# Performance work log

Hardware: AMD Instinct MI355X
Metric: run time of the kernel (lower is better)

The kernel has to match this reference:

```python
import jax, jax.numpy as jnp
import numpy as np

L = 2          # n_layer
H = 8          # n_head
DM = 512       # d_model
DFF = 2048     # d_ff
DH = DM // H   # head dim (query_dimensions)
M = DH         # Favor n_dims random features
B, S = 1, 2048
EPS = 1e-6     # causal linear attention eps
LN_EPS = 1e-5  # torch LayerNorm default


def setup_inputs() -> dict:
    key = jax.random.key(0)
    ks = jax.random.split(key, 12)
    sc = 0.02
    d = {}
    d['x'] = jax.random.normal(ks[0], (B, S, DM), dtype=jnp.float32)
    for i, (n, shape) in enumerate([('Wq', (L, DM, DM)), ('Wk', (L, DM, DM)),
                                    ('Wv', (L, DM, DM)), ('Wo', (L, DM, DM)),
                                    ('W1', (L, DM, DFF)), ('W2', (L, DFF, DM))]):
        d[n] = jax.random.normal(ks[i + 1], shape, dtype=jnp.float32) * sc
    d['bq'] = jnp.zeros((L, DM), jnp.float32)
    d['bk'] = jnp.zeros((L, DM), jnp.float32)
    d['bv'] = jnp.zeros((L, DM), jnp.float32)
    d['bo'] = jnp.zeros((L, DM), jnp.float32)
    d['b1'] = jnp.zeros((L, DFF), jnp.float32)
    d['b2'] = jnp.zeros((L, DM), jnp.float32)
    d['g1'] = jnp.ones((L, DM), jnp.float32)
    d['be1'] = jnp.zeros((L, DM), jnp.float32)
    d['g2'] = jnp.ones((L, DM), jnp.float32)
    d['be2'] = jnp.zeros((L, DM), jnp.float32)
    # FAVOR+ random projection matrix per layer: [Dh, M]
    d['omega'] = jax.random.normal(ks[7], (L, DH, M), dtype=jnp.float32)
    return d


def _favor(x, omega):
    # x: [B,S,H,Dh]; softmax_temp = 1/sqrt(Dh) applied as x * sqrt(temp)
    xs = x * (DH ** -0.25)
    nrm = jnp.sum(xs * xs, axis=-1, keepdims=True)       # [B,S,H,1]
    u = jnp.einsum('bshd,dm->bshm', xs, omega)           # [B,S,H,M]
    return jnp.exp(u - 0.5 * nrm) * (M ** -0.5)


def _ln(x, g, b):
    mu = jnp.mean(x, -1, keepdims=True)
    var = jnp.mean((x - mu) ** 2, -1, keepdims=True)
    return (x - mu) * jax.lax.rsqrt(var + LN_EPS) * g + b


def _forward(x, Wq, bq, Wk, bk, Wv, bv, Wo, bo, omega,
             W1, b1, W2, b2, g1, be1, g2, be2):
    out = x
    for l in range(L):
        q = (out @ Wq[l] + bq[l]).reshape(B, S, H, DH)
        k = (out @ Wk[l] + bk[l]).reshape(B, S, H, DH)
        v = (out @ Wv[l] + bv[l]).reshape(B, S, H, DH)
        pq = _favor(q, omega[l])
        pk = _favor(k, omega[l])
        # causal linear attention: running sums of phi(k) v^T and phi(k)
        kv = jnp.cumsum(jnp.einsum('bshm,bshd->bshmd', pk, v), axis=1)  # [B,S,H,M,Dh]
        num = jnp.einsum('bshm,bshmd->bshd', pq, kv)
        den = jnp.einsum('bshm,bshm->bsh', pq, jnp.cumsum(pk, axis=1)) + EPS
        a = (num / den[..., None]).reshape(B, S, DM)
        # post-norm encoder layer (fast-transformers TransformerEncoderLayer)
        out = out + (a @ Wo[l] + bo[l])
        out = _ln(out, g1[l], be1[l])
        y = jax.nn.relu(out @ W1[l] + b1[l]) @ W2[l] + b2[l]
        out = _ln(out + y, g2[l], be2[l])
    return out


def reference(x, Wq, bq, Wk, bk, Wv, bv, Wo, bo, omega,
              W1, b1, W2, b2, g1, be1, g2, be2):
    return _forward(x, Wq, bq, Wk, bk, Wv, bv, Wo, bo, omega,
                    W1, b1, W2, b2, g1, be1, g2, be2)
```

## Files before the change

kernel.cpp:

```cpp
#include <hip/hip_runtime.h>
#include <hip/hip_bf16.h>

#define S_  2048
#define DM_ 512
#define H_  8
#define DH_ 64
#define MF_ 64
#define DFF_ 2048
#define L_  2
#define CT_ 64
#define NC_ (S_ / CT_)
#define EPS_ 1e-6f
#define LN_EPS_ 1e-5f

#define LSW_   3145728
#define W1OFF_ 1048576
#define W2OFF_ 2097152
#define WOOFF_ 786432

typedef unsigned short ushortT;
typedef unsigned int u32;
typedef float f4 __attribute__((ext_vector_type(4)));
typedef short s8 __attribute__((ext_vector_type(8)));
typedef u32 u32x2 __attribute__((ext_vector_type(2)));

__device__ __forceinline__ ushortT f2b(float f) {
  union { float f; unsigned u; } v; v.f = f;
  unsigned r = v.u + 0x7fffu + ((v.u >> 16) & 1u);
  return (ushortT)(r >> 16);
}
__device__ __forceinline__ float bu2f(ushortT h) {
  union { unsigned u; float f; } v; v.u = ((unsigned)h) << 16; return v.f;
}
__device__ __forceinline__ u32 pk2(float a, float b) {
  return (u32)f2b(a) | ((u32)f2b(b) << 16);
}

__global__ __launch_bounds__(256) void tcast_all(
    const float* __restrict__ x,
    const float* __restrict__ Wq, const float* __restrict__ Wk,
    const float* __restrict__ Wv, const float* __restrict__ Wo,
    const float* __restrict__ W1, const float* __restrict__ W2,
    const float* __restrict__ omg,
    float* __restrict__ cur, ushortT* __restrict__ curb,
    ushortT* __restrict__ wb, ushortT* __restrict__ omgTb) {
  const int bid = blockIdx.x;
  const int t = threadIdx.x;
  if (bid >= 6152) {
    const int i = (bid - 6152) * 256 + t;
    float v = x[i];
    cur[i] = v;
    curb[i] = f2b(v);
    return;
  }
  __shared__ ushortT tile[32][33];
  const float* src; ushortT* dst; int K, N, bx, by;
  if (bid < 2048) {
    const int z = bid >> 8, widx = z & 3, lay = z >> 2;
    const float* s4[4] = {Wq, Wk, Wv, Wo};
    src = s4[widx] + (size_t)lay * DM_ * DM_;
    dst = wb + (size_t)lay * LSW_ + (size_t)widx * DM_ * DM_;
    K = DM_; N = DM_; bx = bid & 15; by = (bid >> 4) & 15;
  } else if (bid < 4096) {
    const int r = bid - 2048;
    const int lay = r >> 10;
    src = W1 + (size_t)lay * DM_ * DFF_;
    dst = wb + (size_t)lay * LSW_ + W1OFF_;
    K = DM_; N = DFF_; bx = r & 63; by = (r >> 6) & 15;
  } else if (bid < 6144) {
    const int r = bid - 4096;
    const int lay = r >> 10;
    src = W2 + (size_t)lay * DFF_ * DM_;
    dst = wb + (size_t)lay * LSW_ + W2OFF_;
    K = DFF_; N = DM_; bx = r & 15; by = (r >> 4) & 63;
  } else {
    const int r = bid - 6144;
    const int lay = r >> 2;
    src = omg + (size_t)lay * DH_ * MF_;
    dst = omgTb + (size_t)lay * DH_ * MF_;
    K = DH_; N = MF_; bx = r & 1; by = (r >> 1) & 1;
  }
  const int cc = t & 31, r0 = t >> 5;
  const int n0 = bx * 32, k0 = by * 32;
#pragma unroll
  for (int i = 0; i < 4; ++i) {
    int r = r0 + 8 * i;
    tile[r][cc] = f2b(src[(size_t)(k0 + r) * N + n0 + cc]);
  }
  __syncthreads();
#pragma unroll
  for (int i = 0; i < 4; ++i) {
    int r = r0 + 8 * i;
    dst[(size_t)(n0 + r) * K + k0 + cc] = tile[cc][r];
  }
}

template<bool RELU, bool HAS_RES, bool OUT_BF16>
__global__ __launch_bounds__(256) void mgemm(
    const ushortT* __restrict__ A, const ushortT* __restrict__ Wt,
    const float* __restrict__ bq_, const float* __restrict__ bk_,
    const float* __restrict__ bv_, const float* __restrict__ Res,
    float* __restrict__ Cf, ushortT* __restrict__ Cb, int K, int N) {
  __shared__ ushortT sA[2][2048];
  __shared__ ushortT sB[2][2048];
  const int t = threadIdx.x;
  const int w = t >> 6, l = t & 63;
  const int wm = w >> 1, wn = w & 1;
  const int n0 = blockIdx.x * 64, m0 = blockIdx.y * 64;
  const int z = blockIdx.z;
  const ushortT* Wz = Wt + (size_t)z * K * N;
  const float* bias = (z == 0) ? bq_ : (z == 1 ? bk_ : bv_);

  const int rs = w * 16 + (l >> 2);
  const int qs = (l & 3) ^ ((rs >> 1) & 3);
  const ushortT* gA = A  + (size_t)(m0 + rs) * K + qs * 8;
  const ushortT* gB = Wz + (size_t)(n0 + rs) * K + qs * 8;

  const int Ra = wm * 32 + (l & 15);
  const int Rb = wn * 32 + (l & 15);
  const int qq = l >> 4;
  const int aoff = (Ra * 4 + (qq ^ ((Ra >> 1) & 3))) * 8;
  const int boff = (Rb * 4 + (qq ^ ((Rb >> 1) & 3))) * 8;

  f4 acc[2][2];
#pragma unroll
  for (int i = 0; i < 2; ++i)
#pragma unroll
    for (int j = 0; j < 2; ++j) acc[i][j] = (f4){0.f, 0.f, 0.f, 0.f};

  auto stage = [&](int buf, int ko) {
    __builtin_amdgcn_global_load_lds(
        (const __attribute__((address_space(1))) void*)(gA + ko),
        (__attribute__((address_space(3))) void*)(&sA[buf][w * 512]), 16, 0, 0);
    __builtin_amdgcn_global_load_lds(
        (const __attribute__((address_space(1))) void*)(gB + ko),
        (__attribute__((address_space(3))) void*)(&sB[buf][w * 512]), 16, 0, 0);
  };

  stage(0, 0);
  const int nk = K >> 5;
  for (int ks = 0; ks < nk; ++ks) {
    __syncthreads();
    if (ks + 1 < nk) stage((ks + 1) & 1, (ks + 1) * 32);
    const ushortT* pa = sA[ks & 1];
    const ushortT* pb = sB[ks & 1];
    s8 a0 = *(const s8*)(pa + aoff);
    s8 a1 = *(const s8*)(pa + aoff + 512);
    s8 b0 = *(const s8*)(pb + boff);
    s8 b1 = *(const s8*)(pb + boff + 512);
    acc[0][0] = __builtin_amdgcn_mfma_f32_16x16x32_bf16(a0, b0, acc[0][0], 0, 0, 0);
    acc[0][1] = __builtin_amdgcn_mfma_f32_16x16x32_bf16(a0, b1, acc[0][1], 0, 0, 0);
    acc[1][0] = __builtin_amdgcn_mfma_f32_16x16x32_bf16(a1, b0, acc[1][0], 0, 0, 0);
    acc[1][1] = __builtin_amdgcn_mfma_f32_16x16x32_bf16(a1, b1, acc[1][1], 0, 0, 0);
  }

  const size_t outz = (size_t)z * S_ * N;
  const int colb = n0 + wn * 32 + (l & 15);
  const int rowb = m0 + wm * 32 + ((l >> 4) << 2);
#pragma unroll
  for (int mt = 0; mt < 2; ++mt) {
#pragma unroll
    for (int nt = 0; nt < 2; ++nt) {
      const int c = colb + nt * 16;
      const float bv = bias[c];
#pragma unroll
      for (int r = 0; r < 4; ++r) {
        const int rr = rowb + mt * 16 + r;
        float v = acc[mt][nt][r] + bv;
        if (HAS_RES) v += Res[(size_t)rr * N + c];
        if (RELU) v = fmaxf(v, 0.f);
        if (OUT_BF16) Cb[outz + (size_t)rr * N + c] = f2b(v);
        else          Cf[outz + (size_t)rr * N + c] = v;
      }
    }
  }
}

__global__ __launch_bounds__(256) void mgemm_part(
    const ushortT* __restrict__ A, const ushortT* __restrict__ Wt,
    float* __restrict__ PS, int K, int N, int KS) {
  __shared__ ushortT sA[2][2048];
  __shared__ ushortT sB[2][2048];
  const int t = threadIdx.x;
  const int w = t >> 6, l = t & 63;
  const int wm = w >> 1, wn = w & 1;
  const int n0 = blockIdx.x * 64, m0 = blockIdx.y * 64;
  const int z = blockIdx.z;

  const int rs = w * 16 + (l >> 2);
  const int qs = (l & 3) ^ ((rs >> 1) & 3);
  const ushortT* gA = A  + (size_t)(m0 + rs) * K + z * KS + qs * 8;
  const ushortT* gB = Wt + (size_t)(n0 + rs) * K + z * KS + qs * 8;

  const int Ra = wm * 32 + (l & 15);
  const int Rb = wn * 32 + (l & 15);
  const int qq = l >> 4;
  const int aoff = (Ra * 4 + (qq ^ ((Ra >> 1) & 3))) * 8;
  const int boff = (Rb * 4 + (qq ^ ((Rb >> 1) & 3))) * 8;

  f4 acc[2][2];
#pragma unroll
  for (int i = 0; i < 2; ++i)
#pragma unroll
    for (int j = 0; j < 2; ++j) acc[i][j] = (f4){0.f, 0.f, 0.f, 0.f};

  auto stage = [&](int buf, int ko) {
    __builtin_amdgcn_global_load_lds(
        (const __attribute__((address_space(1))) void*)(gA + ko),
        (__attribute__((address_space(3))) void*)(&sA[buf][w * 512]), 16, 0, 0);
    __builtin_amdgcn_global_load_lds(
        (const __attribute__((address_space(1))) void*)(gB + ko),
        (__attribute__((address_space(3))) void*)(&sB[buf][w * 512]), 16, 0, 0);
  };

  stage(0, 0);
  const int nk = KS >> 5;
  for (int ks = 0; ks < nk; ++ks) {
    __syncthreads();
    if (ks + 1 < nk) stage((ks + 1) & 1, (ks + 1) * 32);
    const ushortT* pa = sA[ks & 1];
    const ushortT* pb = sB[ks & 1];
    s8 a0 = *(const s8*)(pa + aoff);
    s8 a1 = *(const s8*)(pa + aoff + 512);
    s8 b0 = *(const s8*)(pb + boff);
    s8 b1 = *(const s8*)(pb + boff + 512);
    acc[0][0] = __builtin_amdgcn_mfma_f32_16x16x32_bf16(a0, b0, acc[0][0], 0, 0, 0);
    acc[0][1] = __builtin_amdgcn_mfma_f32_16x16x32_bf16(a0, b1, acc[0][1], 0, 0, 0);
    acc[1][0] = __builtin_amdgcn_mfma_f32_16x16x32_bf16(a1, b0, acc[1][0], 0, 0, 0);
    acc[1][1] = __builtin_amdgcn_mfma_f32_16x16x32_bf16(a1, b1, acc[1][1], 0, 0, 0);
  }

  float* out = PS + (size_t)z * S_ * N;
  const int colb = n0 + wn * 32 + (l & 15);
  const int rowb = m0 + wm * 32 + ((l >> 4) << 2);
#pragma unroll
  for (int mt = 0; mt < 2; ++mt) {
#pragma unroll
    for (int nt = 0; nt < 2; ++nt) {
      const int c = colb + nt * 16;
#pragma unroll
      for (int r = 0; r < 4; ++r)
        out[(size_t)(rowb + mt * 16 + r) * N + c] = acc[mt][nt][r];
    }
  }
}

__global__ __launch_bounds__(256) void redln(const float* __restrict__ PS, int nsplit,
                                             const float* __restrict__ bias,
                                             const float* __restrict__ res,
                                             const float* __restrict__ g,
                                             const float* __restrict__ be,
                                             float* __restrict__ outF,
                                             ushortT* __restrict__ outB) {
  const int s = blockIdx.x, t = threadIdx.x;
  float v0 = bias[t] + res[(size_t)s * DM_ + t];
  float v1 = bias[t + 256] + res[(size_t)s * DM_ + 256 + t];
  for (int z = 0; z < nsplit; ++z) {
    const float* p = PS + (size_t)z * S_ * DM_ + (size_t)s * DM_;
    v0 += p[t];
    v1 += p[256 + t];
  }
  float sum = v0 + v1, sq = v0 * v0 + v1 * v1;
  for (int off = 32; off > 0; off >>= 1) {
    sum += __shfl_down(sum, off);
    sq += __shfl_down(sq, off);
  }
  __shared__ float ssum[4], ssq[4];
  __shared__ float smean, srstd;
  const int w = t >> 6;
  if ((t & 63) == 0) { ssum[w] = sum; ssq[w] = sq; }
  __syncthreads();
  if (t == 0) {
    float S1 = ssum[0] + ssum[1] + ssum[2] + ssum[3];
    float S2 = ssq[0] + ssq[1] + ssq[2] + ssq[3];
    float mu = S1 / DM_;
    smean = mu;
    srstd = rsqrtf(S2 / DM_ - mu * mu + LN_EPS_);
  }
  __syncthreads();
  const float mu = smean, rs = srstd;
  float o0 = (v0 - mu) * rs * g[t] + be[t];
  float o1 = (v1 - mu) * rs * g[256 + t] + be[256 + t];
  outF[(size_t)s * DM_ + t] = o0;
  outF[(size_t)s * DM_ + 256 + t] = o1;
  if (outB) {
    outB[(size_t)s * DM_ + t] = f2b(o0);
    outB[(size_t)s * DM_ + 256 + t] = f2b(o1);
  }
}

__global__ __launch_bounds__(256) void favor_cs(const ushortT* __restrict__ qkv,
                                                const ushortT* __restrict__ omgT,
                                                ushortT* __restrict__ PQb,
                                                ushortT* __restrict__ PKb,
                                                float* __restrict__ KVcT,
                                                float* __restrict__ Kc) {
  const int c = blockIdx.x, h = blockIdx.y, t = threadIdx.x;
  const int w = t >> 6, l = t & 63, lr = l & 15, q = l >> 4;
  __shared__ ushortT xq[64 * 72], xk[64 * 72], vT[64 * 72], omT[64 * 72];
  __shared__ ushortT pq[64 * 72], pk[64 * 72], pkT[64 * 72];
  __shared__ float nrm[128];

  const ushortT* qg = qkv + (size_t)(c * CT_) * DM_ + h * DH_;
  const ushortT* kg = qg + (size_t)S_ * DM_;
  const ushortT* vg = kg + (size_t)S_ * DM_;

  for (int i = t; i < 512; i += 256) {
    const int s = i >> 3, seg = i & 7;
    *(s8*)&xq[s * 72 + seg * 8] = *(const s8*)(qg + (size_t)s * DM_ + seg * 8);
    *(s8*)&xk[s * 72 + seg * 8] = *(const s8*)(kg + (size_t)s * DM_ + seg * 8);
    s8 av = *(const s8*)(vg + (size_t)s * DM_ + seg * 8);
#pragma unroll
    for (int j = 0; j < 8; ++j) vT[(seg * 8 + j) * 72 + s] = (ushortT)av[j];
    *(s8*)&omT[s * 72 + seg * 8] = *(const s8*)(omgT + s * 64 + seg * 8);
  }
  __syncthreads();

  if (t < 128) {
    const ushortT* src = (t < 64) ? xq : xk;
    const int s = t & 63;
    float a = 0.f;
#pragma unroll
    for (int seg = 0; seg < 8; ++seg) {
      s8 vv = *(const s8*)(src + s * 72 + seg * 8);
#pragma unroll
      for (int j = 0; j < 8; ++j) {
        float f = bu2f((ushortT)vv[j]);
        a += f * f;
      }
    }
    nrm[t] = a;
  }
  __syncthreads();

  {
    const float gam = 0.35355339059327373f;
    const int s0 = w * 16;
    s8 aq0 = *(const s8*)&xq[(s0 + lr) * 72 + q * 8];
    s8 aq1 = *(const s8*)&xq[(s0 + lr) * 72 + 32 + q * 8];
    s8 ak0 = *(const s8*)&xk[(s0 + lr) * 72 + q * 8];
    s8 ak1 = *(const s8*)&xk[(s0 + lr) * 72 + 32 + q * 8];
#pragma unroll
    for (int mt = 0; mt < 4; ++mt) {
      s8 b0 = *(const s8*)&omT[(mt * 16 + lr) * 72 + q * 8];
      s8 b1 = *(const s8*)&omT[(mt * 16 + lr) * 72 + 32 + q * 8];
      f4 cq = (f4){0.f, 0.f, 0.f, 0.f}, ck = (f4){0.f, 0.f, 0.f, 0.f};
      cq = __builtin_amdgcn_mfma_f32_16x16x32_bf16(aq0, b0, cq, 0, 0, 0);
      cq = __builtin_amdgcn_mfma_f32_16x16x32_bf16(aq1, b1, cq, 0, 0, 0);
      ck = __builtin_amdgcn_mfma_f32_16x16x32_bf16(ak0, b0, ck, 0, 0, 0);
      ck = __builtin_amdgcn_mfma_f32_16x16x32_bf16(ak1, b1, ck, 0, 0, 0);
#pragma unroll
      for (int r = 0; r < 4; ++r) {
        const int sr = s0 + q * 4 + r, mc = mt * 16 + lr;
        float vq = expf(gam * cq[r] - 0.0625f * nrm[sr]) * 0.125f;
        float vk = expf(gam * ck[r] - 0.0625f * nrm[64 + sr]) * 0.125f;
        pq[sr * 72 + mc] = f2b(vq);
        ushortT hk = f2b(vk);
        pk[sr * 72 + mc] = hk;
        pkT[mc * 72 + sr] = hk;
      }
    }
  }
  __syncthreads();

  {
    const int d0 = w * 16;
    s8 a0 = *(const s8*)&vT[(d0 + lr) * 72 + q * 8];
    s8 a1 = *(const s8*)&vT[(d0 + lr) * 72 + 32 + q * 8];
    float* outb = KVcT + (size_t)(h * NC_ + c) * DH_ * MF_;
#pragma unroll
    for (int mt = 0; mt < 4; ++mt) {
      s8 b0 = *(const s8*)&pkT[(mt * 16 + lr) * 72 + q * 8];
      s8 b1 = *(const s8*)&pkT[(mt * 16 + lr) * 72 + 32 + q * 8];
      f4 cc = (f4){0.f, 0.f, 0.f, 0.f};
      cc = __builtin_amdgcn_mfma_f32_16x16x32_bf16(a0, b0, cc, 0, 0, 0);
      cc = __builtin_amdgcn_mfma_f32_16x16x32_bf16(a1, b1, cc, 0, 0, 0);
#pragma unroll
      for (int r = 0; r < 4; ++r)
        outb[(size_t)(d0 + q * 4 + r) * MF_ + mt * 16 + lr] = cc[r];
    }
  }
  if (t < 64) {
    float s = 0.f;
#pragma unroll
    for (int seg = 0; seg < 8; ++seg) {
      s8 vv = *(const s8*)&pkT[t * 72 + seg * 8];
#pragma unroll
      for (int j = 0; j < 8; ++j) s += bu2f((ushortT)vv[j]);
    }
    Kc[(size_t)(h * NC_ + c) * MF_ + t] = s;
  }
  for (int i = t; i < 512; i += 256) {
    const int s = i >> 3, seg = i & 7;
    *(s8*)(PQb + (size_t)(c * CT_ + s) * DM_ + h * MF_ + seg * 8) = *(const s8*)&pq[s * 72 + seg * 8];
    *(s8*)(PKb + (size_t)(c * CT_ + s) * DM_ + h * MF_ + seg * 8) = *(const s8*)&pk[s * 72 + seg * 8];
  }
}

__global__ __launch_bounds__(256) void attn_pfx(const ushortT* __restrict__ PQ,
                                                const ushortT* __restrict__ PK,
                                                const ushortT* __restrict__ V,
                                                const float* __restrict__ KVcT,
                                                const float* __restrict__ Kc,
                                                ushortT* __restrict__ Aout) {
  const int cc = blockIdx.x, h = blockIdx.y, t = threadIdx.x;
  const int w = t >> 6, l = t & 63;
  const int lr = l & 15, q = l >> 4;

  __shared__ ushortT pqs[64 * 72];
  __shared__ ushortT pks[64 * 72];
  __shared__ ushortT vts[64 * 72];
  __shared__ ushortT kvs[64 * 72];
  __shared__ ushortT tms[64 * 72];
  __shared__ float dpart[256];
  __shared__ float den[64];
  __shared__ float kcs[64];

  const int s0j = t >> 3, seg0 = t & 7;
  const int s1j = (t + 256) >> 3, seg1 = t & 7;
  float acc0[8], acc1[8];
#pragma unroll
  for (int j = 0; j < 8; ++j) { acc0[j] = 0.f; acc1[j] = 0.f; }

  const float* kvbase = KVcT + (size_t)(h * NC_) * DH_ * MF_;
  for (int cp = 0; cp < cc; ++cp) {
    const float* kr = kvbase + (size_t)cp * DH_ * MF_;
    f4 a0 = *(const f4*)(kr + s0j * MF_ + seg0 * 8);
    f4 a1 = *(const f4*)(kr + s0j * MF_ + seg0 * 8 + 4);
    f4 b0 = *(const f4*)(kr + s1j * MF_ + seg1 * 8);
    f4 b1 = *(const f4*)(kr + s1j * MF_ + seg1 * 8 + 4);
    acc0[0] += a0.x; acc0[1] += a0.y; acc0[2] += a0.z; acc0[3] += a0.w;
    acc0[4] += a1.x; acc0[5] += a1.y; acc0[6] += a1.z; acc0[7] += a1.w;
    acc1[0] += b0.x; acc1[1] += b0.y; acc1[2] += b0.z; acc1[3] += b0.w;
    acc1[4] += b1.x; acc1[5] += b1.y; acc1[6] += b1.z; acc1[7] += b1.w;
  }
  {
    u32* p0 = (u32*)&kvs[s0j * 72 + seg0 * 8];
    p0[0] = pk2(acc0[0], acc0[1]); p0[1] = pk2(acc0[2], acc0[3]);
    p0[2] = pk2(acc0[4], acc0[5]); p0[3] = pk2(acc0[6], acc0[7]);
    u32* p1 = (u32*)&kvs[s1j * 72 + seg1 * 8];
    p1[0] = pk2(acc1[0], acc1[1]); p1[1] = pk2(acc1[2], acc1[3]);
    p1[2] = pk2(acc1[4], acc1[5]); p1[3] = pk2(acc1[6], acc1[7]);
  }
  if (t < 64) {
    float s = 0.f;
    for (int cp = 0; cp < cc; ++cp) s += Kc[(size_t)(h * NC_ + cp) * MF_ + t];
    kcs[t] = s;
  }

  for (int i = t; i < 512; i += 256) {
    const int s = i >> 3, seg = i & 7;
    *(s8*)&pqs[s * 72 + seg * 8] = *(const s8*)(PQ + (size_t)(cc * CT_ + s) * DM_ + h * MF_ + seg * 8);
    *(s8*)&pks[s * 72 + seg * 8] = *(const s8*)(PK + (size_t)(cc * CT_ + s) * DM_ + h * MF_ + seg * 8);
    s8 av = *(const s8*)(V + (size_t)(cc * CT_ + s) * DM_ + h * DH_ + seg * 8);
#pragma unroll
    for (int j = 0; j < 8; ++j) vts[(seg * 8 + j) * 72 + s] = (ushortT)av[j];
  }
  __syncthreads();

  {
    const int s0 = w * 16;
    s8 a0 = *(const s8*)&pqs[(s0 + lr) * 72 + q * 8];
    s8 a1 = *(const s8*)&pqs[(s0 + lr) * 72 + 32 + q * 8];
#pragma unroll
    for (int tb = 0; tb < 4; ++tb) {
      f4 c = (f4){0.f, 0.f, 0.f, 0.f};
      if (tb <= w) {
        s8 b0 = *(const s8*)&pks[(tb * 16 + lr) * 72 + q * 8];
        s8 b1 = *(const s8*)&pks[(tb * 16 + lr) * 72 + 32 + q * 8];
        c = __builtin_amdgcn_mfma_f32_16x16x32_bf16(a0, b0, c, 0, 0, 0);
        c = __builtin_amdgcn_mfma_f32_16x16x32_bf16(a1, b1, c, 0, 0, 0);
      }
#pragma unroll
      for (int r = 0; r < 4; ++r) {
        float v = c[r];
        if (tb == w && lr > q * 4 + r) v = 0.f;
        tms[(s0 + q * 4 + r) * 72 + tb * 16 + lr] = f2b(v);
      }
    }
  }
  __syncthreads();

  {
    const int s = t >> 2, part = t & 3;
    float dp = 0.f;
    const u32* trow = (const u32*)&tms[s * 72 + part * 16];
#pragma unroll
    for (int j = 0; j < 8; ++j) {
      u32 u = trow[j];
      dp += bu2f((ushortT)(u & 0xffffu)) + bu2f((ushortT)(u >> 16));
    }
    const u32* qrow = (const u32*)&pqs[s * 72 + part * 16];
    const f4* kc4 = (const f4*)(kcs + part * 16);
#pragma unroll
    for (int j = 0; j < 4; ++j) {
      f4 b = kc4[j];
      u32 ua = qrow[2 * j], ub = qrow[2 * j + 1];
      dp += bu2f((ushortT)(ua & 0xffffu)) * b.x + bu2f((ushortT)(ua >> 16)) * b.y +
            bu2f((ushortT)(ub & 0xffffu)) * b.z + bu2f((ushortT)(ub >> 16)) * b.w;
    }
    dpart[t] = dp;
  }
  __syncthreads();
  if (t < 64)
    den[t] = dpart[4 * t] + dpart[4 * t + 1] + dpart[4 * t + 2] + dpart[4 * t + 3] + EPS_;
  __syncthreads();

  {
    const int d0 = w * 16;
    const int drow = d0 + lr;
    s8 akv0 = *(const s8*)&kvs[drow * 72 + q * 8];
    s8 akv1 = *(const s8*)&kvs[drow * 72 + 32 + q * 8];
    s8 av0  = *(const s8*)&vts[drow * 72 + q * 8];
    s8 av1  = *(const s8*)&vts[drow * 72 + 32 + q * 8];
#pragma unroll
    for (int sb = 0; sb < 4; ++sb) {
      const int srow = sb * 16 + lr;
      s8 bq0 = *(const s8*)&pqs[srow * 72 + q * 8];
      s8 bq1 = *(const s8*)&pqs[srow * 72 + 32 + q * 8];
      s8 bt0 = *(const s8*)&tms[srow * 72 + q * 8];
      s8 bt1 = *(const s8*)&tms[srow * 72 + 32 + q * 8];
      f4 c = (f4){0.f, 0.f, 0.f, 0.f};
      c = __builtin_amdgcn_mfma_f32_16x16x32_bf16(akv0, bq0, c, 0, 0, 0);
      c = __builtin_amdgcn_mfma_f32_16x16x32_bf16(akv1, bq1, c, 0, 0, 0);
      c = __builtin_amdgcn_mfma_f32_16x16x32_bf16(av0, bt0, c, 0, 0, 0);
      c = __builtin_amdgcn_mfma_f32_16x16x32_bf16(av1, bt1, c, 0, 0, 0);
      const float inv = 1.f / den[srow];
      u32x2 o;
      o.x = pk2(c[0] * inv, c[1] * inv);
      o.y = pk2(c[2] * inv, c[3] * inv);
      *(u32x2*)(Aout + (size_t)(cc * CT_ + srow) * DM_ + h * DH_ + d0 + q * 4) = o;
    }
  }
}

extern "C" void kernel_launch(void* const* d_in, const int* in_sizes, int n_in,
                              void* d_out, int out_size, void* d_ws, size_t ws_size,
                              hipStream_t stream) {
  const float* x    = (const float*)d_in[0];
  const float* Wq   = (const float*)d_in[1];
  const float* Wk   = (const float*)d_in[2];
  const float* Wv   = (const float*)d_in[3];
  const float* Wo   = (const float*)d_in[4];
  const float* W1   = (const float*)d_in[5];
  const float* W2   = (const float*)d_in[6];
  const float* bq   = (const float*)d_in[7];
  const float* bk   = (const float*)d_in[8];
  const float* bv   = (const float*)d_in[9];
  const float* bo   = (const float*)d_in[10];
  const float* b1   = (const float*)d_in[11];
  const float* b2   = (const float*)d_in[12];
  const float* g1   = (const float*)d_in[13];
  const float* be1  = (const float*)d_in[14];
  const float* g2   = (const float*)d_in[15];
  const float* be2  = (const float*)d_in[16];
  const float* omg  = (const float*)d_in[17];
  float* out = (float*)d_out;

  const size_t MB = 1048576;
  float* f    = (float*)d_ws;
  float* cur  = f;
  float* ln1  = f + 1 * MB;
  float* KVcb = f + 2 * MB;
  float* Kcb  = f + 3 * MB;
  float* PS   = f + 3 * MB + 16384;

  ushortT* u    = (ushortT*)(f + 8 * MB);
  ushortT* curb = u;
  ushortT* qkb  = u + 1 * MB;
  ushortT* pqb  = u + 4 * MB;
  ushortT* pkb  = u + 5 * MB;
  ushortT* qbb  = u + 6 * MB;
  ushortT* ln1b = u + 7 * MB;
  ushortT* ffb  = u + 8 * MB;
  ushortT* wb   = u + 12 * MB;
  ushortT* omgTb = wb + 2 * LSW_;

  tcast_all<<<10248, 256, 0, stream>>>(x, Wq, Wk, Wv, Wo, W1, W2, omg,
                                       cur, curb, wb, omgTb);

  const dim3 gQKV(DM_ / 64, S_ / 64, 3);
  const dim3 gFF1(DFF_ / 64, S_ / 64, 1);
  const dim3 gWo(DM_ / 64, S_ / 64, 2);
  const dim3 gW2(DM_ / 64, S_ / 64, 4);
  const dim3 gAttn(NC_, H_);

  for (int l = 0; l < L_; ++l) {
    const ushortT* wl = wb + (size_t)l * LSW_;
    const size_t bo512 = (size_t)l * DM_;
    const size_t boFF = (size_t)l * DFF_;

    mgemm<false, false, true><<<gQKV, 256, 0, stream>>>(
        curb, wl, bq + bo512, bk + bo512, bv + bo512, nullptr, nullptr, qkb, DM_, DM_);

    favor_cs<<<gAttn, 256, 0, stream>>>(qkb, omgTb + (size_t)l * DH_ * MF_,
                                        pqb, pkb, KVcb, Kcb);
    attn_pfx<<<gAttn, 256, 0, stream>>>(pqb, pkb, qkb + 2 * (size_t)S_ * DM_,
                                        KVcb, Kcb, qbb);

    mgemm_part<<<gWo, 256, 0, stream>>>(qbb, wl + WOOFF_, PS, DM_, DM_, 256);
    redln<<<S_, 256, 0, stream>>>(PS, 2, bo + bo512, cur, g1 + bo512, be1 + bo512, ln1, ln1b);

    mgemm<true, false, true><<<gFF1, 256, 0, stream>>>(
        ln1b, wl + W1OFF_, b1 + boFF, nullptr, nullptr, nullptr, nullptr, ffb, DM_, DFF_);

    mgemm_part<<<gW2, 256, 0, stream>>>(ffb, wl + W2OFF_, PS, DFF_, DM_, 512);
    const bool last = (l == L_ - 1);
    redln<<<S_, 256, 0, stream>>>(PS, 4, b2 + bo512, ln1, g2 + bo512, be2 + bo512,
                                  last ? out : cur, last ? nullptr : curb);
  }
}
```

Before: 264.8 us.

## Use 128x128 MFMA tiles for FFN GEMMs and precompute attention chunk prefixes

Adds a 128x128-tile MFMA GEMM kernel with a 4x4 accumulator grid per wave and uses it for the W1 (bias+ReLU, bf16 output) and split-K W2 GEMMs. The goal is more data reuse per LDS load and fewer blocks. Separately, a new prefix2 kernel turns the per-chunk KV and K sums into an exclusive prefix scan in place. The attention kernel then loads one prefix chunk instead of looping over all earlier chunks, which removes quadratic redundant global reads. The trade-offs are one extra launch, higher register pressure in the big-tile GEMM, and fewer blocks to fill the GPU.

```diff
diff --git a/kernel.cpp b/kernel.cpp
--- a/kernel.cpp
+++ b/kernel.cpp
@@ -95,11 +95,11 @@
   }
 }
 
-template<bool RELU, bool HAS_RES, bool OUT_BF16>
+template<bool OUT_BF16>
 __global__ __launch_bounds__(256) void mgemm(
     const ushortT* __restrict__ A, const ushortT* __restrict__ Wt,
     const float* __restrict__ bq_, const float* __restrict__ bk_,
-    const float* __restrict__ bv_, const float* __restrict__ Res,
+    const float* __restrict__ bv_,
     float* __restrict__ Cf, ushortT* __restrict__ Cb, int K, int N) {
   __shared__ ushortT sA[2][2048];
   __shared__ ushortT sB[2][2048];
@@ -167,8 +167,6 @@
       for (int r = 0; r < 4; ++r) {
         const int rr = rowb + mt * 16 + r;
         float v = acc[mt][nt][r] + bv;
-        if (HAS_RES) v += Res[(size_t)rr * N + c];
-        if (RELU) v = fmaxf(v, 0.f);
         if (OUT_BF16) Cb[outz + (size_t)rr * N + c] = f2b(v);
         else          Cf[outz + (size_t)rr * N + c] = v;
       }
@@ -245,6 +243,107 @@
   }
 }
 
+template<bool FULL>
+__global__ __launch_bounds__(256) void mgemm128(
+    const ushortT* __restrict__ A, const ushortT* __restrict__ Wt,
+    const float* __restrict__ bias, float* __restrict__ PS,
+    ushortT* __restrict__ Cb, int K, int N, int KS) {
+  __shared__ ushortT sA[2][4096];
+  __shared__ ushortT sB[2][4096];
+  const int t = threadIdx.x;
+  const int w = t >> 6, l = t & 63, lr = l & 15, q = l >> 4;
+  const int wm = w >> 1, wn = w & 1;
+  const int n0 = blockIdx.x * 128, m0 = blockIdx.y * 128;
+  const int z = blockIdx.z;
+
+  const int s0 = w * 128 + l, s1 = s0 + 64;
+  const int r0 = s0 >> 2, kq0 = (s0 & 3) ^ ((r0 >> 1) & 3);
+  const int r1 = s1 >> 2, kq1 = (s1 & 3) ^ ((r1 >> 1) & 3);
+  const ushortT* gA0 = A  + (size_t)(m0 + r0) * K + z * KS + kq0 * 8;
+  const ushortT* gA1 = A  + (size_t)(m0 + r1) * K + z * KS + kq1 * 8;
+  const ushortT* gB0 = Wt + (size_t)(n0 + r0) * K + z * KS + kq0 * 8;
+  const ushortT* gB1 = Wt + (size_t)(n0 + r1) * K + z * KS + kq1 * 8;
+
+  int aoff[4], boff[4];
+#pragma unroll
+  for (int i = 0; i < 4; ++i) {
+    const int RA = wm * 64 + i * 16 + lr;
+    const int RB = wn * 64 + i * 16 + lr;
+    aoff[i] = (RA * 4 + (q ^ ((RA >> 1) & 3))) * 8;
+    boff[i] = (RB * 4 + (q ^ ((RB >> 1) & 3))) * 8;
+  }
+
+  f4 acc[4][4];
+#pragma unroll
+  for (int i = 0; i < 4; ++i)
+#pragma unroll
+    for (int j = 0; j < 4; ++j) acc[i][j] = (f4){0.f, 0.f, 0.f, 0.f};
+
+  auto stage = [&](int buf, int ko) {
+    __builtin_amdgcn_global_load_lds(
+        (const __attribute__((address_space(1))) void*)(gA0 + ko),
+        (__attribute__((address_space(3))) void*)(&sA[buf][w * 1024]), 16, 0, 0);
+    __builtin_amdgcn_global_load_lds(
+        (const __attribute__((address_space(1))) void*)(gA1 + ko),
+        (__attribute__((address_space(3))) void*)(&sA[buf][w * 1024 + 512]), 16, 0, 0);
+    __builtin_amdgcn_global_load_lds(
+        (const __attribute__((address_space(1))) void*)(gB0 + ko),
+        (__attribute__((address_space(3))) void*)(&sB[buf][w * 1024]), 16, 0, 0);
+    __builtin_amdgcn_global_load_lds(
+        (const __attribute__((address_space(1))) void*)(gB1 + ko),
+        (__attribute__((address_space(3))) void*)(&sB[buf][w * 1024 + 512]), 16, 0, 0);
+  };
+
+  stage(0, 0);
+  const int nk = (FULL ? K : KS) >> 5;
+  for (int ks = 0; ks < nk; ++ks) {
+    __syncthreads();
+    if (ks + 1 < nk) stage((ks + 1) & 1, (ks + 1) * 32);
+    const ushortT* pa = sA[ks & 1];
+    const ushortT* pb = sB[ks & 1];
+    s8 a[4], b[4];
+#pragma unroll
+    for (int i = 0; i < 4; ++i) {
+      a[i] = *(const s8*)(pa + aoff[i]);
+      b[i] = *(const s8*)(pb + boff[i]);
+    }
+#pragma unroll
+    for (int mt = 0; mt < 4; ++mt)
+#pragma unroll
+      for (int nt = 0; nt < 4; ++nt)
+        acc[mt][nt] = __builtin_amdgcn_mfma_f32_16x16x32_bf16(a[mt], b[nt], acc[mt][nt], 0, 0, 0);
+  }
+
+  const int colb = n0 + wn * 64 + lr;
+  const int rowb = m0 + wm * 64 + q * 4;
+  if (FULL) {
+#pragma unroll
+    for (int nt = 0; nt < 4; ++nt) {
+      const int c = colb + nt * 16;
+      const float bv = bias[c];
+#pragma unroll
+      for (int mt = 0; mt < 4; ++mt) {
+#pragma unroll
+        for (int r = 0; r < 4; ++r) {
+          const int rr = rowb + mt * 16 + r;
+          Cb[(size_t)rr * N + c] = f2b(fmaxf(acc[mt][nt][r] + bv, 0.f));
+        }
+      }
+    }
+  } else {
+    float* out = PS + (size_t)z * S_ * N;
+#pragma unroll
+    for (int mt = 0; mt < 4; ++mt)
+#pragma unroll
+      for (int nt = 0; nt < 4; ++nt) {
+        const int c = colb + nt * 16;
+#pragma unroll
+        for (int r = 0; r < 4; ++r)
+          out[(size_t)(rowb + mt * 16 + r) * N + c] = acc[mt][nt][r];
+      }
+  }
+}
+
 __global__ __launch_bounds__(256) void redln(const float* __restrict__ PS, int nsplit,
                                              const float* __restrict__ bias,
                                              const float* __restrict__ res,
@@ -397,12 +496,42 @@
   }
 }
 
-__global__ __launch_bounds__(256) void attn_pfx(const ushortT* __restrict__ PQ,
-                                                const ushortT* __restrict__ PK,
-                                                const ushortT* __restrict__ V,
-                                                const float* __restrict__ KVcT,
-                                                const float* __restrict__ Kc,
-                                                ushortT* __restrict__ Aout) {
+__global__ __launch_bounds__(256) void prefix2(float* __restrict__ KVc,
+                                               float* __restrict__ Kc) {
+  const int h = blockIdx.x, seg = blockIdx.y, t = threadIdx.x;
+  if (seg < 16) {
+    float* base = KVc + (size_t)h * NC_ * MF_ * DH_ + seg * 256 + t;
+    float v[NC_];
+#pragma unroll
+    for (int c = 0; c < NC_; ++c) v[c] = base[(size_t)c * MF_ * DH_];
+    float run = 0.f;
+#pragma unroll
+    for (int c = 0; c < NC_; ++c) {
+      float tmp = v[c];
+      base[(size_t)c * MF_ * DH_] = run;
+      run += tmp;
+    }
+  } else if (t < MF_) {
+    float* base = Kc + (size_t)h * NC_ * MF_ + t;
+    float v[NC_];
+#pragma unroll
+    for (int c = 0; c < NC_; ++c) v[c] = base[(size_t)c * MF_];
+    float run = 0.f;
+#pragma unroll
+    for (int c = 0; c < NC_; ++c) {
+      float tmp = v[c];
+      base[(size_t)c * MF_] = run;
+      run += tmp;
+    }
+  }
+}
+
+__global__ __launch_bounds__(256) void attn_mfma(const ushortT* __restrict__ PQ,
+                                                 const ushortT* __restrict__ PK,
+                                                 const ushortT* __restrict__ V,
+                                                 const float* __restrict__ KVcT,
+                                                 const float* __restrict__ Kc,
+                                                 ushortT* __restrict__ Aout) {
   const int cc = blockIdx.x, h = blockIdx.y, t = threadIdx.x;
   const int w = t >> 6, l = t & 63;
   const int lr = l & 15, q = l >> 4;
@@ -414,39 +543,6 @@
   __shared__ ushortT tms[64 * 72];
   __shared__ float dpart[256];
   __shared__ float den[64];
-  __shared__ float kcs[64];
-
-  const int s0j = t >> 3, seg0 = t & 7;
-  const int s1j = (t + 256) >> 3, seg1 = t & 7;
-  float acc0[8], acc1[8];
-#pragma unroll
-  for (int j = 0; j < 8; ++j) { acc0[j] = 0.f; acc1[j] = 0.f; }
-
-  const float* kvbase = KVcT + (size_t)(h * NC_) * DH_ * MF_;
-  for (int cp = 0; cp < cc; ++cp) {
-    const float* kr = kvbase + (size_t)cp * DH_ * MF_;
-    f4 a0 = *(const f4*)(kr + s0j * MF_ + seg0 * 8);
-    f4 a1 = *(const f4*)(kr + s0j * MF_ + seg0 * 8 + 4);
-    f4 b0 = *(const f4*)(kr + s1j * MF_ + seg1 * 8);
-    f4 b1 = *(const f4*)(kr + s1j * MF_ + seg1 * 8 + 4);
-    acc0[0] += a0.x; acc0[1] += a0.y; acc0[2] += a0.z; acc0[3] += a0.w;
-    acc0[4] += a1.x; acc0[5] += a1.y; acc0[6] += a1.z; acc0[7] += a1.w;
-    acc1[0] += b0.x; acc1[1] += b0.y; acc1[2] += b0.z; acc1[3] += b0.w;
-    acc1[4] += b1.x; acc1[5] += b1.y; acc1[6] += b1.z; acc1[7] += b1.w;
-  }
-  {
-    u32* p0 = (u32*)&kvs[s0j * 72 + seg0 * 8];
-    p0[0] = pk2(acc0[0], acc0[1]); p0[1] = pk2(acc0[2], acc0[3]);
-    p0[2] = pk2(acc0[4], acc0[5]); p0[3] = pk2(acc0[6], acc0[7]);
-    u32* p1 = (u32*)&kvs[s1j * 72 + seg1 * 8];
-    p1[0] = pk2(acc1[0], acc1[1]); p1[1] = pk2(acc1[2], acc1[3]);
-    p1[2] = pk2(acc1[4], acc1[5]); p1[3] = pk2(acc1[6], acc1[7]);
-  }
-  if (t < 64) {
-    float s = 0.f;
-    for (int cp = 0; cp < cc; ++cp) s += Kc[(size_t)(h * NC_ + cp) * MF_ + t];
-    kcs[t] = s;
-  }
 
   for (int i = t; i < 512; i += 256) {
     const int s = i >> 3, seg = i & 7;
@@ -455,6 +551,12 @@
     s8 av = *(const s8*)(V + (size_t)(cc * CT_ + s) * DM_ + h * DH_ + seg * 8);
 #pragma unroll
     for (int j = 0; j < 8; ++j) vts[(seg * 8 + j) * 72 + s] = (ushortT)av[j];
+    const float* kr = KVcT + (size_t)((h * NC_ + cc) * DH_ + s) * MF_ + seg * 8;
+    f4 g0 = *(const f4*)kr;
+    f4 g1 = *(const f4*)(kr + 4);
+    u32* p = (u32*)&kvs[s * 72 + seg * 8];
+    p[0] = pk2(g0.x, g0.y); p[1] = pk2(g0.z, g0.w);
+    p[2] = pk2(g1.x, g1.y); p[3] = pk2(g1.z, g1.w);
   }
   __syncthreads();
 
@@ -491,7 +593,7 @@
       dp += bu2f((ushortT)(u & 0xffffu)) + bu2f((ushortT)(u >> 16));
     }
     const u32* qrow = (const u32*)&pqs[s * 72 + part * 16];
-    const f4* kc4 = (const f4*)(kcs + part * 16);
+    const f4* kc4 = (const f4*)(Kc + (size_t)(h * NC_ + cc) * MF_ + part * 16);
 #pragma unroll
     for (int j = 0; j < 4; ++j) {
       f4 b = kc4[j];
@@ -580,31 +682,34 @@
                                        cur, curb, wb, omgTb);
 
   const dim3 gQKV(DM_ / 64, S_ / 64, 3);
-  const dim3 gFF1(DFF_ / 64, S_ / 64, 1);
   const dim3 gWo(DM_ / 64, S_ / 64, 2);
-  const dim3 gW2(DM_ / 64, S_ / 64, 4);
+  const dim3 gW1(DFF_ / 128, S_ / 128, 1);
+  const dim3 gW2(DM_ / 128, S_ / 128, 4);
   const dim3 gAttn(NC_, H_);
+  const dim3 gPre(H_, 17);
 
   for (int l = 0; l < L_; ++l) {
     const ushortT* wl = wb + (size_t)l * LSW_;
     const size_t bo512 = (size_t)l * DM_;
     const size_t boFF = (size_t)l * DFF_;
 
-    mgemm<false, false, true><<<gQKV, 256, 0, stream>>>(
-        curb, wl, bq + bo512, bk + bo512, bv + bo512, nullptr, nullptr, qkb, DM_, DM_);
+    mgemm<true><<<gQKV, 256, 0, stream>>>(
+        curb, wl, bq + bo512, bk + bo512, bv + bo512, nullptr, qkb, DM_, DM_);
 
     favor_cs<<<gAttn, 256, 0, stream>>>(qkb, omgTb + (size_t)l * DH_ * MF_,
                                         pqb, pkb, KVcb, Kcb);
-    attn_pfx<<<gAttn, 256, 0, stream>>>(pqb, pkb, qkb + 2 * (size_t)S_ * DM_,
-                                        KVcb, Kcb, qbb);
+    prefix2<<<gPre, 256, 0, stream>>>(KVcb, Kcb);
+    attn_mfma<<<gAttn, 256, 0, stream>>>(pqb, pkb, qkb + 2 * (size_t)S_ * DM_,
+                                         KVcb, Kcb, qbb);
 
     mgemm_part<<<gWo, 256, 0, stream>>>(qbb, wl + WOOFF_, PS, DM_, DM_, 256);
     redln<<<S_, 256, 0, stream>>>(PS, 2, bo + bo512, cur, g1 + bo512, be1 + bo512, ln1, ln1b);
 
-    mgemm<true, false, true><<<gFF1, 256, 0, stream>>>(
-        ln1b, wl + W1OFF_, b1 + boFF, nullptr, nullptr, nullptr, nullptr, ffb, DM_, DFF_);
-
-    mgemm_part<<<gW2, 256, 0, stream>>>(ffb, wl + W2OFF_, PS, DFF_, DM_, 512);
+    mgemm128<true><<<gW1, 256, 0, stream>>>(
+        ln1b, wl + W1OFF_, b1 + boFF, nullptr, ffb, DM_, DFF_, 0);
+
+    mgemm128<false><<<gW2, 256, 0, stream>>>(
+        ffb, wl + W2OFF_, nullptr, PS, nullptr, DFF_, DM_, 512);
     const bool last = (l == L_ - 1);
     redln<<<S_, 256, 0, stream>>>(PS, 4, b2 + bo512, ln1, g2 + bo512, be2 + bo512,
                                   last ? out : cur, last ? nullptr : curb);
```

New measurement: 249.5 us. -5.8%, faster.
